# Optimization experiments

Measured on AMD Instinct MI355X. Metric: run time of the kernel, lower is better.

Reference implementation:

```python
import jax, jax.numpy as jnp
import numpy as np

B, M, N = 8, 1024, 2048          # batch, check nodes, variable nodes
NUM_ITERS = 5
ROW_DEGREE = 8                   # ones per check row (sparse Tanner graph)
NEG_BIG = -1e30 - 1.0


def _make_H():
    rng = np.random.RandomState(0)
    H = np.zeros((M, N), dtype=np.int32)
    for i in range(M):
        cols = rng.choice(N, size=ROW_DEGREE, replace=False)
        H[i, cols] = 1
    # guarantee every variable node has at least one check
    empty = np.where(H.sum(0) == 0)[0]
    for j in empty:
        H[rng.randint(M), j] = 1
    return H


def setup_inputs() -> dict:
    key = jax.random.key(0)
    k1, _ = jax.random.split(key)
    soft_input = jax.random.normal(k1, (B, N), dtype=jnp.float32) * 2.0
    check_weight = jnp.full((1,), -1.07, dtype=jnp.float32)  # NMS normalized factor
    H = jnp.asarray(_make_H())
    return {"soft_input": soft_input, "check_weight": check_weight, "H": H}


def reference(soft_input, check_weight, H):
    Hf = H.astype(jnp.float32)                      # [M, N]
    back = jnp.where(Hf == 0, NEG_BIG, 0.0)[None]   # [1, M, N]
    supp = (1.0 - Hf)[None]                         # [1, M, N]
    alpha = jax.nn.softplus(check_weight)           # NMS scalar normalization

    def body(cv, _):
        # --- variable-to-check: vc = (sum_m cv + llr) on edges, minus own message
        col_sum = jnp.sum(cv, axis=1) + soft_input            # [B, N]
        vc = col_sum[:, None, :] * Hf - cv                    # [B, M, N]
        # --- check-to-variable: min-sum with min/submin trick
        vc_abs = jnp.clip(jnp.abs(vc), 0.0, 1e30)
        dec = -vc_abs + back                                  # mask off non-edges
        top2 = jax.lax.top_k(dec, 2)[0]                       # [B, M, 2]
        mn = (-top2[..., 0])[:, :, None] * Hf                 # row min, broadcast on edges
        sub = (-top2[..., 1])[:, :, None] * Hf                # row second min
        result = jnp.where(vc_abs > mn, mn, sub)              # exclude-self min
        sign = jnp.sign(supp + vc)                            # non-edges -> sign(+1)
        row_prod = jnp.prod(sign, axis=2)[:, :, None] * Hf
        result_sign = row_prod * sign                         # product of other signs
        cv_new = result * jax.lax.stop_gradient(result_sign) * alpha
        return cv_new, None

    cv0 = jnp.zeros((soft_input.shape[0], Hf.shape[0], Hf.shape[1]), jnp.float32)
    cv_final, _ = jax.lax.scan(body, cv0, None, length=NUM_ITERS)
    soft_output = soft_input + jnp.sum(cv_final, axis=1)      # [B, N] posterior LLRs
    return soft_output
```

## Files before the change

### kernel.cpp

```cpp
#include <hip/hip_runtime.h>
#include <hip/hip_bf16.h>


#define M_CHECK 1024
#define N_VAR   2048
#define BATCH   8
#define MAXD    12
#define NUM_ITERS 5
#define FXS 16384.0f
#define FXI (1.0f / 16384.0f)

__global__ __launch_bounds__(256) void build_rows_kernel(
    const int* __restrict__ H, int* __restrict__ deg,
    int* __restrict__ row_cols_T)
{
    const int m    = blockIdx.x * 4 + (threadIdx.x >> 6);
    const int lane = threadIdx.x & 63;
    const unsigned long long below = (1ULL << lane) - 1ULL;
    const int4* __restrict__ H4 = (const int4*)(H + m * N_VAR);

    int base = 0;
    for (int c = 0; c < N_VAR; c += 256) {
        int4 h = H4[(c >> 2) + lane];
        unsigned long long m0 = __ballot(h.x != 0);
        unsigned long long m1 = __ballot(h.y != 0);
        unsigned long long m2 = __ballot(h.z != 0);
        unsigned long long m3 = __ballot(h.w != 0);
        int pb = __popcll(m0 & below) + __popcll(m1 & below)
               + __popcll(m2 & below) + __popcll(m3 & below);
        int b0 = (int)((m0 >> lane) & 1);
        int b1 = (int)((m1 >> lane) & 1);
        int b2 = (int)((m2 >> lane) & 1);
        int col = c + 4 * lane;
        int r = base + pb;
        if (h.x) { if (r < MAXD) row_cols_T[r * M_CHECK + m] = col; }
        r += b0;
        if (h.y) { if (r < MAXD) row_cols_T[r * M_CHECK + m] = col + 1; }
        r += b1;
        if (h.z) { if (r < MAXD) row_cols_T[r * M_CHECK + m] = col + 2; }
        r += b2;
        if (h.w) { if (r < MAXD) row_cols_T[r * M_CHECK + m] = col + 3; }
        base += __popcll(m0) + __popcll(m1) + __popcll(m2) + __popcll(m3);
    }
    if (lane == 0) deg[m] = (base < MAXD) ? base : MAXD;
}

#define ROW_BODY(DLIM, PRED, ACCG, ACCS, PEEL)                               \
  {                                                                          \
    float vcs[MAXD];                                                         \
    float mn1 = 1e38f, mn2 = 1e38f;                                          \
    unsigned sx = 0u; bool zr = false;                                       \
    _Pragma("unroll")                                                        \
    for (int d = 0; d < DLIM; ++d) {                                         \
      if (!PRED || d < dm) {                                                 \
        float vc = PEEL ? softc[d]                                           \
                        : softc[d] + (float)ACCG[cols[d]] * FXI - cv[d];     \
        vcs[d] = vc;                                                         \
        float a = fabsf(vc);                                                 \
        if (a < mn1) { mn2 = mn1; mn1 = a; }                                 \
        else if (a < mn2) { mn2 = a; }                                       \
        sx ^= (__float_as_uint(vc) & 0x80000000u);                           \
        zr |= (vc == 0.f);                                                   \
      }                                                                      \
    }                                                                        \
    const float zmul = zr ? 0.f : alpha;                                     \
    _Pragma("unroll")                                                        \
    for (int d = 0; d < DLIM; ++d) {                                         \
      if (!PRED || d < dm) {                                                 \
        float vc  = vcs[d];                                                  \
        float a   = fabsf(vc);                                               \
        float res = (a > mn1) ? mn1 : mn2;             \
        unsigned o = sx ^ (__float_as_uint(vc) & 0x80000000u);               \
        float v   = res * zmul;                                    \
        float cvn = __uint_as_float(__float_as_uint(v) ^ o);                 \
        cv[d] = cvn;                                                         \
        atomicAdd(&ACCS[cols[d]], __float2int_rn(cvn * FXS));                \
      }                                                                      \
    }                                                                        \
  }

#define DECODE_ITER(ACCG, ACCS, PEEL, DO_RESET, ACCR)                        \
  if (clean) ROW_BODY(8,    false, ACCG, ACCS, PEEL)                         \
  else       ROW_BODY(MAXD, true,  ACCG, ACCS, PEEL)                         \
  if (DO_RESET) { ACCR[n0] = 0; ACCR[n1] = 0; }                              \
  __syncthreads();

__global__ __launch_bounds__(1024) void decode_kernel(
    const float* __restrict__ soft_input, const float* __restrict__ check_weight,
    const int* __restrict__ deg, const int* __restrict__ row_cols_T,
    float* __restrict__ out)
{
    __shared__ int   acc0[N_VAR];
    __shared__ int   acc1[N_VAR];
    __shared__ int   acc2[N_VAR];
    __shared__ float soft_s[N_VAR];
    __shared__ int   wc[16];

    const int b = blockIdx.x;
    const int t = threadIdx.x;
    const float alpha = log1pf(expf(check_weight[0]));

    const int n0 = t, n1 = t + 1024;
    const float s0 = soft_input[b * N_VAR + n0];
    const float s1 = soft_input[b * N_VAR + n1];
    soft_s[n0] = s0;  soft_s[n1] = s1;
    acc1[n0] = 0; acc1[n1] = 0;
    acc2[n0] = 0; acc2[n1] = 0;

    const int  dmo   = deg[t];
    const bool dirty = (dmo != 8);
    const int  lane  = t & 63, w = t >> 6;
    unsigned long long dmask = __ballot(dirty);
    const int rnk = __popcll(dmask & ((1ULL << lane) - 1ULL));
    if (lane == 0) wc[w] = __popcll(dmask);
    __syncthreads();

    int totd = 0, pref = 0;
#pragma unroll
    for (int i = 0; i < 16; ++i) {
        int c = wc[i];
        totd += c;
        if (i < w) pref += c;
    }
    const int n8 = M_CHECK - totd;
    const int db = pref + rnk;
    const int new_id = dirty ? (n8 + db) : (t - db);
    acc0[new_id] = t;
    __syncthreads();

    const int  orig  = acc0[t];
    const int  dm    = deg[orig];
    const bool clean = ((t | 63) < n8);

    int cols[MAXD];
#pragma unroll
    for (int d = 0; d < MAXD; ++d)
        cols[d] = (d < dm) ? row_cols_T[d * M_CHECK + orig] : 0;

    float softc[MAXD];
#pragma unroll
    for (int d = 0; d < MAXD; ++d)
        softc[d] = (d < dm) ? soft_s[cols[d]] : 0.f;

    float cv[MAXD];

    DECODE_ITER(acc0, acc1,  true,  false, acc0)
    DECODE_ITER(acc1, acc2,  false, true,  acc0)
    DECODE_ITER(acc2, acc0,  false, true,  acc1)
    DECODE_ITER(acc0, acc1,  false, true,  acc2)
    DECODE_ITER(acc1, acc2,  false, false, acc0)

    out[b * N_VAR + n0] = s0 + (float)acc2[n0] * FXI;
    out[b * N_VAR + n1] = s1 + (float)acc2[n1] * FXI;
}

extern "C" void kernel_launch(void* const* d_in, const int* in_sizes, int n_in,
                              void* d_out, int out_size, void* d_ws, size_t ws_size,
                              hipStream_t stream)
{
    const float* soft_input   = (const float*)d_in[0];
    const float* check_weight = (const float*)d_in[1];
    const int*   H            = (const int*)d_in[2];
    float*       out          = (float*)d_out;

    int* deg        = (int*)d_ws;
    int* row_cols_T = deg + M_CHECK;

    build_rows_kernel<<<M_CHECK / 4, 256, 0, stream>>>(H, deg, row_cols_T);
    decode_kernel<<<BATCH, 1024, 0, stream>>>(
        soft_input, check_weight, deg, row_cols_T, out);
}
```

Before: 21.71 us.

## Fuse H parsing and decoding into one launch with flag-based block handoff

```diff
diff --git a/kernel.cpp b/kernel.cpp
--- a/kernel.cpp
+++ b/kernel.cpp
@@ -9,41 +9,9 @@
 #define NUM_ITERS 5
 #define FXS 16384.0f
 #define FXI (1.0f / 16384.0f)
-
-__global__ __launch_bounds__(256) void build_rows_kernel(
-    const int* __restrict__ H, int* __restrict__ deg,
-    int* __restrict__ row_cols_T)
-{
-    const int m    = blockIdx.x * 4 + (threadIdx.x >> 6);
-    const int lane = threadIdx.x & 63;
-    const unsigned long long below = (1ULL << lane) - 1ULL;
-    const int4* __restrict__ H4 = (const int4*)(H + m * N_VAR);
-
-    int base = 0;
-    for (int c = 0; c < N_VAR; c += 256) {
-        int4 h = H4[(c >> 2) + lane];
-        unsigned long long m0 = __ballot(h.x != 0);
-        unsigned long long m1 = __ballot(h.y != 0);
-        unsigned long long m2 = __ballot(h.z != 0);
-        unsigned long long m3 = __ballot(h.w != 0);
-        int pb = __popcll(m0 & below) + __popcll(m1 & below)
-               + __popcll(m2 & below) + __popcll(m3 & below);
-        int b0 = (int)((m0 >> lane) & 1);
-        int b1 = (int)((m1 >> lane) & 1);
-        int b2 = (int)((m2 >> lane) & 1);
-        int col = c + 4 * lane;
-        int r = base + pb;
-        if (h.x) { if (r < MAXD) row_cols_T[r * M_CHECK + m] = col; }
-        r += b0;
-        if (h.y) { if (r < MAXD) row_cols_T[r * M_CHECK + m] = col + 1; }
-        r += b1;
-        if (h.z) { if (r < MAXD) row_cols_T[r * M_CHECK + m] = col + 2; }
-        r += b2;
-        if (h.w) { if (r < MAXD) row_cols_T[r * M_CHECK + m] = col + 3; }
-        base += __popcll(m0) + __popcll(m1) + __popcll(m2) + __popcll(m3);
-    }
-    if (lane == 0) deg[m] = (base < MAXD) ? base : MAXD;
-}
+#define NPARSE 64
+#define ROWS_PER_PARSE (M_CHECK / NPARSE)
+#define FLAG_MAGIC(i) (0x9E3779B9u ^ ((unsigned)(i) * 0x85EBCA6Bu))
 
 #define ROW_BODY(DLIM, PRED, ACCG, ACCS, PEEL)                               \
   {                                                                          \
@@ -85,9 +53,10 @@
   if (DO_RESET) { ACCR[n0] = 0; ACCR[n1] = 0; }                              \
   __syncthreads();
 
-__global__ __launch_bounds__(1024) void decode_kernel(
+__global__ __launch_bounds__(1024) void fused_kernel(
     const float* __restrict__ soft_input, const float* __restrict__ check_weight,
-    const int* __restrict__ deg, const int* __restrict__ row_cols_T,
+    const int* __restrict__ H, unsigned* __restrict__ flags,
+    int* __restrict__ deg, int* __restrict__ row_cols_T,
     float* __restrict__ out)
 {
     __shared__ int   acc0[N_VAR];
@@ -96,7 +65,60 @@
     __shared__ float soft_s[N_VAR];
     __shared__ int   wc[16];
 
-    const int b = blockIdx.x;
+    const int blk = blockIdx.x;
+
+    if (blk >= BATCH) {
+        const int pb   = blk - BATCH;
+        const int w    = threadIdx.x >> 6;
+        const int lane = threadIdx.x & 63;
+        const int m    = pb * ROWS_PER_PARSE + w;
+        const unsigned long long below = (1ULL << lane) - 1ULL;
+        const int4* __restrict__ H4 = (const int4*)(H + m * N_VAR);
+
+        int base = 0;
+        for (int c = 0; c < N_VAR; c += 256) {
+            int4 h = H4[(c >> 2) + lane];
+            unsigned long long m0 = __ballot(h.x != 0);
+            unsigned long long m1 = __ballot(h.y != 0);
+            unsigned long long m2 = __ballot(h.z != 0);
+            unsigned long long m3 = __ballot(h.w != 0);
+            int pbel = __popcll(m0 & below) + __popcll(m1 & below)
+                     + __popcll(m2 & below) + __popcll(m3 & below);
+            int b0 = (int)((m0 >> lane) & 1);
+            int b1 = (int)((m1 >> lane) & 1);
+            int b2 = (int)((m2 >> lane) & 1);
+            int col = c + 4 * lane;
+            int r = base + pbel;
+            if (h.x) { if (r < MAXD) row_cols_T[r * M_CHECK + m] = col; }
+            r += b0;
+            if (h.y) { if (r < MAXD) row_cols_T[r * M_CHECK + m] = col + 1; }
+            r += b1;
+            if (h.z) { if (r < MAXD) row_cols_T[r * M_CHECK + m] = col + 2; }
+            r += b2;
+            if (h.w) { if (r < MAXD) row_cols_T[r * M_CHECK + m] = col + 3; }
+            base += __popcll(m0) + __popcll(m1) + __popcll(m2) + __popcll(m3);
+        }
+        if (lane == 0) deg[m] = (base < MAXD) ? base : MAXD;
+
+        __syncthreads();
+        if (threadIdx.x == 0) {
+            __threadfence();
+            __hip_atomic_store(&flags[pb], FLAG_MAGIC(pb),
+                               __ATOMIC_RELEASE, __HIP_MEMORY_SCOPE_AGENT);
+        }
+        return;
+    }
+
+    if (threadIdx.x < NPARSE) {
+        const unsigned want = FLAG_MAGIC(threadIdx.x);
+        while (__hip_atomic_load(&flags[threadIdx.x],
+                                 __ATOMIC_ACQUIRE, __HIP_MEMORY_SCOPE_AGENT)
+               != want) { }
+    }
+    __syncthreads();
+    __threadfence();
+
+    const int b = blk;
     const int t = threadIdx.x;
     const float alpha = log1pf(expf(check_weight[0]));
 
@@ -163,10 +185,10 @@
     const int*   H            = (const int*)d_in[2];
     float*       out          = (float*)d_out;
 
-    int* deg        = (int*)d_ws;
-    int* row_cols_T = deg + M_CHECK;
+    unsigned* flags      = (unsigned*)d_ws;
+    int*      deg        = (int*)d_ws + 64;
+    int*      row_cols_T = deg + M_CHECK;
 
-    build_rows_kernel<<<M_CHECK / 4, 256, 0, stream>>>(H, deg, row_cols_T);
-    decode_kernel<<<BATCH, 1024, 0, stream>>>(
-        soft_input, check_weight, deg, row_cols_T, out);
+    fused_kernel<<<BATCH + NPARSE, 1024, 0, stream>>>(
+        soft_input, check_weight, H, flags, deg, row_cols_T, out);
 }
```

New measurement: 25.35 us. +16.8%, slower.
